# Kernel optimization log

Measured on AMD Instinct MI355X. Metric: run time of the kernel, lower is better.

Reference implementation:

```python
import jax, jax.numpy as jnp
import numpy as np

B, D, H, C, T, F = 4096, 1024, 2048, 1000, 819200, 32


def setup_inputs() -> dict:
    key = jax.random.key(0)
    ks = jax.random.split(key, 12)
    feature_vector = jax.random.normal(ks[0], (B, D), dtype=jnp.float32)
    var_flat = jax.random.normal(ks[1], (T, F), dtype=jnp.float32)
    segment_ids = jnp.sort(jax.random.randint(ks[2], (T,), 0, B))
    target_vector = jax.random.randint(ks[3], (B,), 0, C)
    target_scalar = jax.random.normal(ks[4], (B,), dtype=jnp.float32)
    # learned params (torch Linear convention: W [out, in])
    Wv = jax.random.normal(ks[5], (D, F), dtype=jnp.float32) / np.sqrt(F)
    bv = jnp.zeros((D,), dtype=jnp.float32)
    W1 = jax.random.normal(ks[6], (H, D), dtype=jnp.float32) / np.sqrt(D)
    b1 = jnp.zeros((H,), dtype=jnp.float32)
    W2 = jax.random.normal(ks[7], (C, H), dtype=jnp.float32) / np.sqrt(H)
    b2 = jnp.zeros((C,), dtype=jnp.float32)
    Ws = jax.random.normal(ks[8], (1, H), dtype=jnp.float32) / np.sqrt(H)
    bs = jnp.zeros((1,), dtype=jnp.float32)
    return {
        "feature_vector": feature_vector, "var_flat": var_flat,
        "segment_ids": segment_ids, "target_vector": target_vector,
        "target_scalar": target_scalar, "Wv": Wv, "bv": bv,
        "W1": W1, "b1": b1, "W2": W2, "b2": b2, "Ws": Ws, "bs": bs,
    }


def reference(feature_vector, var_flat, segment_ids, target_vector, target_scalar,
              Wv, bv, W1, b1, W2, b2, Ws, bs):
    nb = feature_vector.shape[0]
    # ragged per-item mean via segment reduce (replaces python loop)
    sums = jax.ops.segment_sum(var_flat, segment_ids, num_segments=nb)      # [B, 32]
    counts = jax.ops.segment_sum(jnp.ones((var_flat.shape[0],), var_flat.dtype),
                                 segment_ids, num_segments=nb)
    means = sums / jnp.maximum(counts, 1.0)[:, None]
    var_processed = means @ Wv.T + bv                                        # [B, D]
    combined = feature_vector + var_processed
    hidden = jax.nn.relu(combined @ W1.T + b1)                               # [B, H]
    vector_output = hidden @ W2.T + b2                                       # [B, C]
    scalar_output = (hidden @ Ws.T + bs).squeeze(-1)                         # [B]
    logp = jax.nn.log_softmax(vector_output, axis=-1)
    loss_vector = -jnp.mean(jnp.take_along_axis(logp, target_vector[:, None], axis=1))
    loss_scalar = jnp.mean(jnp.square(scalar_output - target_scalar))
    total_loss = loss_vector + loss_scalar
    acc = jnp.mean((jnp.argmax(vector_output, axis=1) == target_vector).astype(jnp.float32))
    return total_loss, loss_vector, loss_scalar, acc
```

## Files before the change

kernel.cpp:

```cpp
#include <hip/hip_runtime.h>
#include <hip/hip_bf16.h>
#include <math.h>

#define B_  4096
#define D_  1024
#define H_  2048
#define C_  1000
#define T_  819200
#define F_  32
#define NPAD2 1024
#define NPART 1024

typedef __attribute__((ext_vector_type(8))) short short8;
typedef __attribute__((ext_vector_type(4))) float f32x4;

static const size_t WS_MEANS    = 0;
static const size_t WS_PV       = WS_MEANS + (size_t)B_ * F_ * 4;
static const size_t WS_PA       = WS_PV + NPART * 4;
static const size_t WS_PS       = WS_PA + NPART * 4;
static const size_t WS_B2P      = WS_PS + NPART * 4;
static const size_t WS_COMBINED = 1u << 20;
static const size_t WS_W1BF     = WS_COMBINED + (size_t)B_ * D_ * 2;
static const size_t WS_W2BF     = WS_W1BF + (size_t)H_ * D_ * 2;
static const size_t WS_HIDDEN   = WS_W2BF + (size_t)NPAD2 * H_ * 2;
static const size_t WS_LOGITS   = WS_HIDDEN + (size_t)B_ * H_ * 2;

#define PREP_BLOCKS (B_ + 1024 + 1024 + 4)
__global__ __launch_bounds__(256) void prep_kernel(
    const float* __restrict__ var_flat, const int* __restrict__ seg_ids,
    float* __restrict__ means,
    const float* __restrict__ W1, __hip_bfloat16* __restrict__ W1oct,
    const float* __restrict__ W2, const float* __restrict__ Wsc,
    __hip_bfloat16* __restrict__ W2oct,
    const float* __restrict__ b2, const float* __restrict__ bsc,
    float* __restrict__ b2p) {
  const int id  = blockIdx.x;
  const int tid = threadIdx.x;

  if (id < B_) {
    const int seg = id;
    __shared__ int bounds[2];
    __shared__ float red[4][8][4];
    if (tid < 2) {
      int tgt = seg + tid;
      int lo = 0, hi = T_;
      while (lo < hi) {
        int mid = (lo + hi) >> 1;
        if (seg_ids[mid] < tgt) lo = mid + 1; else hi = mid;
      }
      bounds[tid] = lo;
    }
    __syncthreads();
    const int start = bounds[0], end = bounds[1];
    const int cnt = end - start;
    const int c4 = (tid & 7) * 4;
    const int rl = tid >> 3;
    float a0 = 0.f, a1 = 0.f, a2 = 0.f, a3 = 0.f;
    for (int r = start + rl; r < end; r += 32) {
      float4 v = *(const float4*)(var_flat + (size_t)r * F_ + c4);
      a0 += v.x; a1 += v.y; a2 += v.z; a3 += v.w;
    }
#pragma unroll
    for (int o = 8; o < 64; o <<= 1) {
      a0 += __shfl_down(a0, o, 64);
      a1 += __shfl_down(a1, o, 64);
      a2 += __shfl_down(a2, o, 64);
      a3 += __shfl_down(a3, o, 64);
    }
    const int w = tid >> 6, lane = tid & 63;
    if (lane < 8) {
      red[w][lane][0] = a0; red[w][lane][1] = a1;
      red[w][lane][2] = a2; red[w][lane][3] = a3;
    }
    __syncthreads();
    if (tid < 32) {
      int cg = tid >> 2, e = tid & 3;
      float s = red[0][cg][e] + red[1][cg][e] + red[2][cg][e] + red[3][cg][e];
      float inv = cnt > 0 ? 1.f / (float)cnt : 0.f;
      means[(size_t)seg * F_ + cg * 4 + e] = s * inv;
    }
    return;
  }

  if (id < B_ + 1024) {
    int t = id - B_;
    int bx = t & 15, by = t >> 4;
    int d0 = bx * 64, n0 = by * 32;
    int n_l = tid >> 3, kc = tid & 7;
    int n = n0 + n_l;
    int dd = d0 + kc * 8;
    float4 a = *(const float4*)(W1 + (size_t)n * D_ + dd);
    float4 b = *(const float4*)(W1 + (size_t)n * D_ + dd + 4);
    __hip_bfloat16 tb[8];
    tb[0] = __float2bfloat16(a.x); tb[1] = __float2bfloat16(a.y);
    tb[2] = __float2bfloat16(a.z); tb[3] = __float2bfloat16(a.w);
    tb[4] = __float2bfloat16(b.x); tb[5] = __float2bfloat16(b.y);
    tb[6] = __float2bfloat16(b.z); tb[7] = __float2bfloat16(b.w);
    *(uint4*)(W1oct + ((size_t)(bx * 8 + kc) * H_ + n) * 8) = *(uint4*)tb;
    return;
  }

  if (id < B_ + 2048) {
    int t = id - B_ - 1024;
    int bx = t & 31, by = t >> 5;
    int h0 = bx * 64, n0 = by * 32;
    int n_l = tid >> 3, kc = tid & 7;
    int n = n0 + n_l;
    int hh = h0 + kc * 8;
    float va[8] = {0.f, 0.f, 0.f, 0.f, 0.f, 0.f, 0.f, 0.f};
    const float* src = nullptr;
    if (n < C_)       src = W2 + (size_t)n * H_ + hh;
    else if (n == C_) src = Wsc + hh;
    if (src) {
      float4 a = *(const float4*)(src);
      float4 b = *(const float4*)(src + 4);
      va[0] = a.x; va[1] = a.y; va[2] = a.z; va[3] = a.w;
      va[4] = b.x; va[5] = b.y; va[6] = b.z; va[7] = b.w;
    }
    __hip_bfloat16 tb[8];
#pragma unroll
    for (int e = 0; e < 8; ++e) tb[e] = __float2bfloat16(va[e]);
    *(uint4*)(W2oct + ((size_t)(bx * 8 + kc) * NPAD2 + n) * 8) = *(uint4*)tb;
    return;
  }

  {
    int i = (id - B_ - 2048) * 256 + tid;
    float v = 0.f;
    if (i < C_) v = b2[i];
    else if (i == C_) v = bsc[0];
    b2p[i] = v;
  }
}

__global__ __launch_bounds__(256) void combined_kernel(
    const float* __restrict__ feat, const float* __restrict__ means,
    const float* __restrict__ Wv, const float* __restrict__ bv,
    __hip_bfloat16* __restrict__ comb_oct) {
  __shared__ float m_s[32][F_ + 1];
  __shared__ float wv_s[64][F_ + 1];
  int tid = threadIdx.x;
  int d0 = blockIdx.x * 64;
  int b0 = blockIdx.y * 32;
  {
    int b_l = tid >> 3, f4 = (tid & 7) * 4;
    float4 s4 = *(const float4*)(means + (size_t)(b0 + b_l) * F_ + f4);
    m_s[b_l][f4 + 0] = s4.x; m_s[b_l][f4 + 1] = s4.y;
    m_s[b_l][f4 + 2] = s4.z; m_s[b_l][f4 + 3] = s4.w;
  }
  {
    int r = tid >> 2, p = (tid & 3) * 8;
    float4 a = *(const float4*)(Wv + (size_t)(d0 + r) * F_ + p);
    float4 b = *(const float4*)(Wv + (size_t)(d0 + r) * F_ + p + 4);
    wv_s[r][p + 0] = a.x; wv_s[r][p + 1] = a.y; wv_s[r][p + 2] = a.z; wv_s[r][p + 3] = a.w;
    wv_s[r][p + 4] = b.x; wv_s[r][p + 5] = b.y; wv_s[r][p + 6] = b.z; wv_s[r][p + 7] = b.w;
  }
  __syncthreads();
  int b_l = tid >> 3, kc = tid & 7;
  int b = b0 + b_l;
  int dbase = d0 + kc * 8;
  float4 f0 = *(const float4*)(feat + (size_t)b * D_ + dbase);
  float4 f1 = *(const float4*)(feat + (size_t)b * D_ + dbase + 4);
  float4 v0 = *(const float4*)(bv + dbase);
  float4 v1 = *(const float4*)(bv + dbase + 4);
  float fv[8]  = {f0.x, f0.y, f0.z, f0.w, f1.x, f1.y, f1.z, f1.w};
  float bvv[8] = {v0.x, v0.y, v0.z, v0.w, v1.x, v1.y, v1.z, v1.w};
  __hip_bfloat16 outv[8];
#pragma unroll
  for (int e = 0; e < 8; ++e) {
    float acc = fv[e] + bvv[e];
    const float* wr = wv_s[kc * 8 + e];
#pragma unroll
    for (int f = 0; f < F_; ++f) acc = fmaf(m_s[b_l][f], wr[f], acc);
    outv[e] = __float2bfloat16(acc);
  }
  *(uint4*)(comb_oct + ((size_t)(blockIdx.x * 8 + kc) * B_ + b) * 8) = *(uint4*)outv;
}

__device__ inline void load16_lds(const short* g, short* l) {
  __builtin_amdgcn_global_load_lds(
      (const __attribute__((address_space(1))) void*)g,
      (__attribute__((address_space(3))) void*)l, 16, 0, 0);
}

template <int MODE>
__global__ __launch_bounds__(256) void gemm_mfma_kernel(
    const short* __restrict__ A, const short* __restrict__ Bm,
    const float* __restrict__ bias, void* __restrict__ Cout,
    int M, int Nrows, int K, int Nout) {
  __shared__ short As[2][2048];
  __shared__ short Bs[2][4096];
  const int tid  = threadIdx.x;
  const int lane = tid & 63;
  const int w    = tid >> 6;
  const int bm = blockIdx.y * 64;
  const int bn = blockIdx.x * 128;
  const int wm = (w >> 1) * 32;
  const int wn = (w & 1) * 64;
  const int m_lane = lane & 15;
  const int quad   = lane >> 4;

  f32x4 acc[2][4];
#pragma unroll
  for (int i = 0; i < 2; ++i)
#pragma unroll
    for (int j = 0; j < 4; ++j) acc[i][j] = f32x4{0.f, 0.f, 0.f, 0.f};

  const size_t strideA = (size_t)M * 32;
  const size_t strideB = (size_t)Nrows * 32;
  const short* pA  = A  + ((size_t)w * M + bm) * 8 + lane * 8;
  const short* pB0 = Bm + ((size_t)w * Nrows + bn) * 8 + lane * 8;
  const short* pB1 = pB0 + 64 * 8;
  const int lA  = w * 512;
  const int lB0 = w * 1024;
  const int lB1 = lB0 + 512;

  load16_lds(pA,  &As[0][lA]);
  load16_lds(pB0, &Bs[0][lB0]);
  load16_lds(pB1, &Bs[0][lB1]);

  const int iters = K >> 5;
  for (int it = 0; it < iters; ++it) {
    const int cur = it & 1, nxt = cur ^ 1;
    __syncthreads();
    if (it + 1 < iters) {
      pA += strideA; pB0 += strideB; pB1 += strideB;
      load16_lds(pA,  &As[nxt][lA]);
      load16_lds(pB0, &Bs[nxt][lB0]);
      load16_lds(pB1, &Bs[nxt][lB1]);
    }
    short8 af[2], bf[4];
#pragma unroll
    for (int i = 0; i < 2; ++i)
      af[i] = *(const short8*)&As[cur][quad * 512 + (wm + i * 16 + m_lane) * 8];
#pragma unroll
    for (int j = 0; j < 4; ++j)
      bf[j] = *(const short8*)&Bs[cur][quad * 1024 + (wn + j * 16 + m_lane) * 8];
#pragma unroll
    for (int i = 0; i < 2; ++i)
#pragma unroll
      for (int j = 0; j < 4; ++j)
        acc[i][j] = __builtin_amdgcn_mfma_f32_16x16x32_bf16(af[i], bf[j], acc[i][j], 0, 0, 0);
  }

  const int row0 = bm + wm + quad * 4;
  const int col0 = bn + wn + m_lane;
  if (MODE == 0) {
    __hip_bfloat16* Cb = (__hip_bfloat16*)Cout;
#pragma unroll
    for (int j = 0; j < 4; ++j) {
      int col = col0 + j * 16;
      float bsv = bias[col];
      __hip_bfloat16* base = Cb + ((size_t)(col >> 3) * M) * 8 + (col & 7);
#pragma unroll
      for (int i = 0; i < 2; ++i)
#pragma unroll
        for (int r = 0; r < 4; ++r) {
          int row = row0 + i * 16 + r;
          float v = acc[i][j][r] + bsv;
          v = v > 0.f ? v : 0.f;
          base[(size_t)row * 8] = __float2bfloat16(v);
        }
    }
  } else {
    float* Cf = (float*)Cout;
#pragma unroll
    for (int j = 0; j < 4; ++j) {
      int col = col0 + j * 16;
      float bsv = bias[col];
#pragma unroll
      for (int i = 0; i < 2; ++i)
#pragma unroll
        for (int r = 0; r < 4; ++r) {
          int row = row0 + i * 16 + r;
          Cf[(size_t)row * Nout + col] = acc[i][j][r] + bsv;
        }
    }
  }
}

__global__ __launch_bounds__(256) void loss_kernel(
    const float* __restrict__ logits, const int* __restrict__ target,
    const float* __restrict__ tgt_scal,
    float* __restrict__ pv, float* __restrict__ pa, float* __restrict__ ps) {
  int tid  = threadIdx.x;
  int lane = tid & 63;
  int w    = tid >> 6;
  int b    = blockIdx.x * 4 + w;
  const float*  row  = logits + (size_t)b * NPAD2;
  const float4* row4 = (const float4*)row;
  float v[16];
  float vmax = -INFINITY;
  int   imax = 0x7fffffff;
#pragma unroll
  for (int k = 0; k < 4; ++k) {
    int c4 = lane + 64 * k;
    float4 x = row4[c4];
    float e0 = x.x, e1 = x.y, e2 = x.z, e3 = x.w;
    int idx = c4 * 4;
    if (idx + 0 >= C_) e0 = -INFINITY;
    if (idx + 1 >= C_) e1 = -INFINITY;
    if (idx + 2 >= C_) e2 = -INFINITY;
    if (idx + 3 >= C_) e3 = -INFINITY;
    v[k * 4 + 0] = e0; v[k * 4 + 1] = e1; v[k * 4 + 2] = e2; v[k * 4 + 3] = e3;
    if (e0 > vmax) { vmax = e0; imax = idx + 0; }
    if (e1 > vmax) { vmax = e1; imax = idx + 1; }
    if (e2 > vmax) { vmax = e2; imax = idx + 2; }
    if (e3 > vmax) { vmax = e3; imax = idx + 3; }
  }
#pragma unroll
  for (int o = 32; o > 0; o >>= 1) {
    float ov = __shfl_down(vmax, o, 64);
    int   oi = __shfl_down(imax, o, 64);
    if (ov > vmax || (ov == vmax && oi < imax)) { vmax = ov; imax = oi; }
  }
  vmax = __shfl(vmax, 0, 64);
  float se = 0.f;
#pragma unroll
  for (int j = 0; j < 16; ++j) se += expf(v[j] - vmax);
#pragma unroll
  for (int o = 32; o > 0; o >>= 1) se += __shfl_down(se, o, 64);
  __shared__ float s_nll[4], s_acc[4], s_sq[4];
  if (lane == 0) {
    int t = target[b];
    float logp = row[t] - vmax - logf(se);
    s_nll[w] = -logp;
    s_acc[w] = (imax == t) ? 1.f : 0.f;
    float d = row[C_] - tgt_scal[b];
    s_sq[w] = d * d;
  }
  __syncthreads();
  if (tid == 0) {
    pv[blockIdx.x] = s_nll[0] + s_nll[1] + s_nll[2] + s_nll[3];
    pa[blockIdx.x] = s_acc[0] + s_acc[1] + s_acc[2] + s_acc[3];
    ps[blockIdx.x] = s_sq[0] + s_sq[1] + s_sq[2] + s_sq[3];
  }
}

__global__ __launch_bounds__(256) void finalize_kernel(
    const float* __restrict__ pv, const float* __restrict__ pa,
    const float* __restrict__ ps, float* __restrict__ out) {
  int tid  = threadIdx.x;
  int lane = tid & 63;
  int w    = tid >> 6;
  float nll = 0.f, acc = 0.f, sq = 0.f;
  for (int i = tid; i < NPART; i += 256) {
    nll += pv[i]; acc += pa[i]; sq += ps[i];
  }
#pragma unroll
  for (int o = 32; o > 0; o >>= 1) {
    nll += __shfl_down(nll, o, 64);
    acc += __shfl_down(acc, o, 64);
    sq  += __shfl_down(sq,  o, 64);
  }
  __shared__ float sn[4], sa[4], ss[4];
  if (lane == 0) { sn[w] = nll; sa[w] = acc; ss[w] = sq; }
  __syncthreads();
  if (tid == 0) {
    float lv = (sn[0] + sn[1] + sn[2] + sn[3]) * (1.f / B_);
    float ls = (ss[0] + ss[1] + ss[2] + ss[3]) * (1.f / B_);
    float ac = (sa[0] + sa[1] + sa[2] + sa[3]) * (1.f / B_);
    out[0] = lv + ls;
    out[1] = lv;
    out[2] = ls;
    out[3] = ac;
  }
}

extern "C" void kernel_launch(void* const* d_in, const int* in_sizes, int n_in,
                              void* d_out, int out_size, void* d_ws, size_t ws_size,
                              hipStream_t stream) {
  const float* feature  = (const float*)d_in[0];
  const float* var_flat = (const float*)d_in[1];
  const int*   seg_ids  = (const int*)d_in[2];
  const int*   tgt_vec  = (const int*)d_in[3];
  const float* tgt_scal = (const float*)d_in[4];
  const float* Wv = (const float*)d_in[5];
  const float* bv = (const float*)d_in[6];
  const float* W1 = (const float*)d_in[7];
  const float* b1 = (const float*)d_in[8];
  const float* W2 = (const float*)d_in[9];
  const float* b2 = (const float*)d_in[10];
  const float* Ws = (const float*)d_in[11];
  const float* bs = (const float*)d_in[12];
  float* out = (float*)d_out;

  char* ws = (char*)d_ws;
  float* means  = (float*)(ws + WS_MEANS);
  float* pv     = (float*)(ws + WS_PV);
  float* pa     = (float*)(ws + WS_PA);
  float* ps     = (float*)(ws + WS_PS);
  float* b2p    = (float*)(ws + WS_B2P);
  __hip_bfloat16* comb_oct = (__hip_bfloat16*)(ws + WS_COMBINED);
  __hip_bfloat16* W1oct    = (__hip_bfloat16*)(ws + WS_W1BF);
  __hip_bfloat16* W2oct    = (__hip_bfloat16*)(ws + WS_W2BF);
  __hip_bfloat16* hid_oct  = (__hip_bfloat16*)(ws + WS_HIDDEN);
  float*          logits   = (float*)(ws + WS_LOGITS);

  prep_kernel<<<PREP_BLOCKS, 256, 0, stream>>>(
      var_flat, seg_ids, means, W1, W1oct, W2, Ws, W2oct, b2, bs, b2p);

  {
    dim3 grid(D_ / 64, B_ / 32);
    combined_kernel<<<grid, 256, 0, stream>>>(feature, means, Wv, bv, comb_oct);
  }

  {
    dim3 grid(H_ / 128, B_ / 64);
    gemm_mfma_kernel<0><<<grid, 256, 0, stream>>>(
        (const short*)comb_oct, (const short*)W1oct, b1, hid_oct, B_, H_, D_, H_);
  }

  {
    dim3 grid(NPAD2 / 128, B_ / 64);
    gemm_mfma_kernel<1><<<grid, 256, 0, stream>>>(
        (const short*)hid_oct, (const short*)W2oct, b2p, logits, B_, NPAD2, H_, NPAD2);
  }

  loss_kernel<<<B_ / 4, 256, 0, stream>>>(logits, tgt_vec, tgt_scal, pv, pa, ps);

  finalize_kernel<<<1, 256, 0, stream>>>(pv, pa, ps, out);
}
```

Measured before the change: 295.4 us.

## Precompute segment starts in separate kernel; reorder prep blocks and unroll segment sum

A new kernel scans the sorted segment ids once and writes each segment's start offset into the workspace. This replaces the per-block binary search over 819200 ids that each segment-mean block used to run before it could begin. The segment-mean blocks now come after the weight-conversion blocks in the prep grid, and the row accumulation uses two independent accumulators to raise memory-level parallelism. The cost is an extra kernel launch plus a full pass over segment_ids (about 3.2 MB read).

```diff
diff --git a/kernel.cpp b/kernel.cpp
--- a/kernel.cpp
+++ b/kernel.cpp
@@ -19,15 +19,27 @@
 static const size_t WS_PA       = WS_PV + NPART * 4;
 static const size_t WS_PS       = WS_PA + NPART * 4;
 static const size_t WS_B2P      = WS_PS + NPART * 4;
+static const size_t WS_STARTS   = WS_B2P + NPAD2 * 4;
 static const size_t WS_COMBINED = 1u << 20;
 static const size_t WS_W1BF     = WS_COMBINED + (size_t)B_ * D_ * 2;
 static const size_t WS_W2BF     = WS_W1BF + (size_t)H_ * D_ * 2;
 static const size_t WS_HIDDEN   = WS_W2BF + (size_t)NPAD2 * H_ * 2;
 static const size_t WS_LOGITS   = WS_HIDDEN + (size_t)B_ * H_ * 2;
 
-#define PREP_BLOCKS (B_ + 1024 + 1024 + 4)
+__global__ __launch_bounds__(256) void bounds_kernel(
+    const int* __restrict__ seg_ids, int* __restrict__ starts) {
+  int i = blockIdx.x * 256 + threadIdx.x;
+  if (i >= T_) return;
+  int cur  = seg_ids[i];
+  int prev = (i == 0) ? -1 : seg_ids[i - 1];
+  for (int s = prev + 1; s <= cur; ++s) starts[s] = i;
+  if (i == T_ - 1)
+    for (int s = cur + 1; s <= B_; ++s) starts[s] = T_;
+}
+
+#define PREP_BLOCKS (1024 + 1024 + 4 + B_)
 __global__ __launch_bounds__(256) void prep_kernel(
-    const float* __restrict__ var_flat, const int* __restrict__ seg_ids,
+    const float* __restrict__ var_flat, const int* __restrict__ starts,
     float* __restrict__ means,
     const float* __restrict__ W1, __hip_bfloat16* __restrict__ W1oct,
     const float* __restrict__ W2, const float* __restrict__ Wsc,
@@ -37,54 +49,8 @@
   const int id  = blockIdx.x;
   const int tid = threadIdx.x;
 
-  if (id < B_) {
-    const int seg = id;
-    __shared__ int bounds[2];
-    __shared__ float red[4][8][4];
-    if (tid < 2) {
-      int tgt = seg + tid;
-      int lo = 0, hi = T_;
-      while (lo < hi) {
-        int mid = (lo + hi) >> 1;
-        if (seg_ids[mid] < tgt) lo = mid + 1; else hi = mid;
-      }
-      bounds[tid] = lo;
-    }
-    __syncthreads();
-    const int start = bounds[0], end = bounds[1];
-    const int cnt = end - start;
-    const int c4 = (tid & 7) * 4;
-    const int rl = tid >> 3;
-    float a0 = 0.f, a1 = 0.f, a2 = 0.f, a3 = 0.f;
-    for (int r = start + rl; r < end; r += 32) {
-      float4 v = *(const float4*)(var_flat + (size_t)r * F_ + c4);
-      a0 += v.x; a1 += v.y; a2 += v.z; a3 += v.w;
-    }
-#pragma unroll
-    for (int o = 8; o < 64; o <<= 1) {
-      a0 += __shfl_down(a0, o, 64);
-      a1 += __shfl_down(a1, o, 64);
-      a2 += __shfl_down(a2, o, 64);
-      a3 += __shfl_down(a3, o, 64);
-    }
-    const int w = tid >> 6, lane = tid & 63;
-    if (lane < 8) {
-      red[w][lane][0] = a0; red[w][lane][1] = a1;
-      red[w][lane][2] = a2; red[w][lane][3] = a3;
-    }
-    __syncthreads();
-    if (tid < 32) {
-      int cg = tid >> 2, e = tid & 3;
-      float s = red[0][cg][e] + red[1][cg][e] + red[2][cg][e] + red[3][cg][e];
-      float inv = cnt > 0 ? 1.f / (float)cnt : 0.f;
-      means[(size_t)seg * F_ + cg * 4 + e] = s * inv;
-    }
-    return;
-  }
-
-  if (id < B_ + 1024) {
-    int t = id - B_;
-    int bx = t & 15, by = t >> 4;
+  if (id < 1024) {
+    int bx = id & 15, by = id >> 4;
     int d0 = bx * 64, n0 = by * 32;
     int n_l = tid >> 3, kc = tid & 7;
     int n = n0 + n_l;
@@ -100,8 +66,8 @@
     return;
   }
 
-  if (id < B_ + 2048) {
-    int t = id - B_ - 1024;
+  if (id < 2048) {
+    int t = id - 1024;
     int bx = t & 31, by = t >> 5;
     int h0 = bx * 64, n0 = by * 32;
     int n_l = tid >> 3, kc = tid & 7;
@@ -124,12 +90,56 @@
     return;
   }
 
-  {
-    int i = (id - B_ - 2048) * 256 + tid;
+  if (id < 2052) {
+    int i = (id - 2048) * 256 + tid;
     float v = 0.f;
     if (i < C_) v = b2[i];
     else if (i == C_) v = bsc[0];
     b2p[i] = v;
+    return;
+  }
+
+  {
+    const int seg = id - 2052;
+    const int start = starts[seg];
+    const int end   = starts[seg + 1];
+    const int cnt = end - start;
+    const int c4 = (tid & 7) * 4;
+    const int rl = tid >> 3;
+    float a0 = 0.f, a1 = 0.f, a2 = 0.f, a3 = 0.f;
+    float b0 = 0.f, b1 = 0.f, b2v = 0.f, b3 = 0.f;
+    int r = start + rl;
+    for (; r + 32 < end; r += 64) {
+      float4 v = *(const float4*)(var_flat + (size_t)r * F_ + c4);
+      float4 u = *(const float4*)(var_flat + (size_t)(r + 32) * F_ + c4);
+      a0 += v.x; a1 += v.y; a2 += v.z; a3 += v.w;
+      b0 += u.x; b1 += u.y; b2v += u.z; b3 += u.w;
+    }
+    if (r < end) {
+      float4 v = *(const float4*)(var_flat + (size_t)r * F_ + c4);
+      a0 += v.x; a1 += v.y; a2 += v.z; a3 += v.w;
+    }
+    a0 += b0; a1 += b1; a2 += b2v; a3 += b3;
+#pragma unroll
+    for (int o = 8; o < 64; o <<= 1) {
+      a0 += __shfl_down(a0, o, 64);
+      a1 += __shfl_down(a1, o, 64);
+      a2 += __shfl_down(a2, o, 64);
+      a3 += __shfl_down(a3, o, 64);
+    }
+    __shared__ float red[4][8][4];
+    const int w = tid >> 6, lane = tid & 63;
+    if (lane < 8) {
+      red[w][lane][0] = a0; red[w][lane][1] = a1;
+      red[w][lane][2] = a2; red[w][lane][3] = a3;
+    }
+    __syncthreads();
+    if (tid < 32) {
+      int cg = tid >> 2, e = tid & 3;
+      float s = red[0][cg][e] + red[1][cg][e] + red[2][cg][e] + red[3][cg][e];
+      float inv = cnt > 0 ? 1.f / (float)cnt : 0.f;
+      means[(size_t)seg * F_ + cg * 4 + e] = s * inv;
+    }
   }
 }
 
@@ -391,14 +401,17 @@
   float* pa     = (float*)(ws + WS_PA);
   float* ps     = (float*)(ws + WS_PS);
   float* b2p    = (float*)(ws + WS_B2P);
+  int*   starts = (int*)(ws + WS_STARTS);
   __hip_bfloat16* comb_oct = (__hip_bfloat16*)(ws + WS_COMBINED);
   __hip_bfloat16* W1oct    = (__hip_bfloat16*)(ws + WS_W1BF);
   __hip_bfloat16* W2oct    = (__hip_bfloat16*)(ws + WS_W2BF);
   __hip_bfloat16* hid_oct  = (__hip_bfloat16*)(ws + WS_HIDDEN);
   float*          logits   = (float*)(ws + WS_LOGITS);
 
+  bounds_kernel<<<(T_ + 255) / 256, 256, 0, stream>>>(seg_ids, starts);
+
   prep_kernel<<<PREP_BLOCKS, 256, 0, stream>>>(
-      var_flat, seg_ids, means, W1, W1oct, W2, Ws, W2oct, b2, bs, b2p);
+      var_flat, starts, means, W1, W1oct, W2, Ws, W2oct, b2, bs, b2p);
 
   {
     dim3 grid(D_ / 64, B_ / 32);
```

New measurement: 284.4 us. -3.7%, faster.
